# Kernel tuning notes

Hardware: AMD Instinct MI355X
Metric: run time of the kernel (lower is better)

The kernel has to match this reference:

```python
import jax, jax.numpy as jnp
import numpy as np

B, LQ, LKV, D = 4, 4096, 256, 1024
H, KVH, HD = 16, 4, 64
ROPE_BASE = 10000.0


def rotate_half(x):
    x1, x2 = jnp.split(x, 2, axis=-1)
    return jnp.concatenate([-x2, x1], axis=-1)


def rope_cos_sin(seq_len, dim, dtype):
    inv_freq = 1.0 / (ROPE_BASE ** (jnp.arange(0, dim, 2, dtype=jnp.float32) / dim))
    t = jnp.arange(seq_len, dtype=jnp.float32)
    freqs = t[:, None] * inv_freq[None, :]            # (T, dim/2)
    emb = jnp.concatenate([freqs, freqs], axis=-1)    # (T, dim)
    return jnp.cos(emb).astype(dtype), jnp.sin(emb).astype(dtype)


def apply_rope_indexed(x, cos, sin, pos_ids):
    # x: (B, L, H, HD); cos/sin: (T, HD); pos_ids: (L,)
    c = cos[pos_ids][None, :, None, :]
    s = sin[pos_ids][None, :, None, :]
    return x * c + rotate_half(x) * s


def setup_inputs() -> dict:
    key = jax.random.key(0)
    ks = jax.random.split(key, 10)
    sd = 1.0 / np.sqrt(D)
    return {
        "patches": jax.random.normal(ks[0], (B, LQ, D), jnp.float32),
        "latents": jax.random.normal(ks[1], (B, LKV, D), jnp.float32),
        "Wq": jax.random.normal(ks[2], (D, H * HD), jnp.float32) * sd,
        "bq": jax.random.normal(ks[3], (H * HD,), jnp.float32) * sd,
        "Wk": jax.random.normal(ks[4], (D, KVH * HD), jnp.float32) * sd,
        "bk": jax.random.normal(ks[5], (KVH * HD,), jnp.float32) * sd,
        "Wv": jax.random.normal(ks[6], (D, KVH * HD), jnp.float32) * sd,
        "bv": jax.random.normal(ks[7], (KVH * HD,), jnp.float32) * sd,
        "Wo": jax.random.normal(ks[8], (D, D), jnp.float32) * sd,
        "bo": jax.random.normal(ks[9], (D,), jnp.float32) * sd,
        "num_frames": 16,
    }


def reference(patches, latents, Wq, bq, Wk, bk, Wv, bv, Wo, bo, num_frames):
    Bc, Lq, C = patches.shape
    Lkv = latents.shape[1]
    q = (patches @ Wq + bq).reshape(Bc, Lq, H, HD)
    k = (latents @ Wk + bk).reshape(Bc, Lkv, KVH, HD)
    v = (latents @ Wv + bv).reshape(Bc, Lkv, KVH, HD)

    if num_frames > 1:
        cos, sin = rope_cos_sin(num_frames, HD, q.dtype)
        q_idx = jnp.arange(Lq) // (Lq // num_frames)
        k_idx = jnp.arange(Lkv) // (Lkv // num_frames)
        q = apply_rope_indexed(q, cos, sin, q_idx)
        k = apply_rope_indexed(k, cos, sin, k_idx)

    # GQA: expand kv heads (repeat_interleave along head axis)
    k = jnp.repeat(k, H // KVH, axis=2)
    v = jnp.repeat(v, H // KVH, axis=2)

    scale = 1.0 / np.sqrt(HD)
    scores = jnp.einsum('bqhd,bkhd->bhqk', q, k) * scale
    probs = jax.nn.softmax(scores, axis=-1)
    out = jnp.einsum('bhqk,bkhd->bqhd', probs, v).reshape(Bc, Lq, C)
    return out @ Wo + bo
```

## Files before the change

kernel.cpp:

```cpp
#include <hip/hip_runtime.h>
#include <hip/hip_fp16.h>
#include <cstdint>

typedef _Float16 f16x8 __attribute__((ext_vector_type(8)));
typedef _Float16 f16x4 __attribute__((ext_vector_type(4)));
typedef float    f32x4 __attribute__((ext_vector_type(4)));
typedef float    f32x16 __attribute__((ext_vector_type(16)));

#define MFMA16(a, b, c) __builtin_amdgcn_mfma_f32_16x16x32_f16((a), (b), (c), 0, 0, 0)
#define MFMA32(a, b, c) __builtin_amdgcn_mfma_f32_32x32x16_f16((a), (b), (c), 0, 0, 0)


__device__ __forceinline__ void async_cp16(const _Float16* g, _Float16* l) {
    __builtin_amdgcn_global_load_lds(
        (const __attribute__((address_space(1))) void*)g,
        (__attribute__((address_space(3))) void*)l, 16, 0, 0);
}

__global__ __launch_bounds__(256) void cvt_all(const float4* __restrict__ patches,
                                               const float4* __restrict__ latents,
                                               f16x4* __restrict__ p16,
                                               f16x4* __restrict__ l16) {
    const long i = (long)blockIdx.x * 256 + threadIdx.x;
    const float4 v = (i < 4194304) ? patches[i] : latents[i - 4194304];
    f16x4 o;
    o[0] = (_Float16)v.x; o[1] = (_Float16)v.y;
    o[2] = (_Float16)v.z; o[3] = (_Float16)v.w;
    if (i < 4194304) p16[i] = o; else l16[i - 4194304] = o;
}

__global__ __launch_bounds__(256) void transpose_all(
    const float* __restrict__ Wq, const float* __restrict__ Wk,
    const float* __restrict__ Wv, const float* __restrict__ Wo,
    _Float16* __restrict__ WqT, _Float16* __restrict__ WkvT,
    _Float16* __restrict__ WoT) {
    const int z = blockIdx.z;
    const float* W;
    _Float16* WT;
    int Nd;
    if (z == 0)      { W = Wq; WT = WqT;                       Nd = 1024; }
    else if (z == 1) { W = Wk; WT = WkvT;                      Nd = 256;  }
    else if (z == 2) { W = Wv; WT = WkvT + (size_t)256 * 1024; Nd = 256;  }
    else             { W = Wo; WT = WoT;                       Nd = 1024; }
    const int n0 = blockIdx.x * 64, k0 = blockIdx.y * 64;
    if (n0 >= Nd) return;

    __shared__ float T[64][65];
    const int tid = threadIdx.x;
    const int nl = tid & 63, kg = tid >> 6;
#pragma unroll
    for (int i = 0; i < 16; ++i) {
        const int kl = kg * 16 + i;
        T[kl][nl] = W[(size_t)(k0 + kl) * Nd + n0 + nl];
    }
    __syncthreads();
    const int kl = tid & 63;
#pragma unroll
    for (int i = 0; i < 16; ++i) {
        const int nl2 = kg * 16 + i;
        WT[(size_t)(n0 + nl2) * 1024 + k0 + kl] = (_Float16)T[kl][nl2];
    }
}

__global__ void catbias(const float* __restrict__ a, const float* __restrict__ b,
                        float* __restrict__ o) {
    const int i = threadIdx.x;
    o[i] = (i < 256) ? a[i] : b[i - 256];
}

template <int EPI>
__global__ __launch_bounds__(256, 2) void gemm32(const _Float16* __restrict__ A,
                                                 const _Float16* __restrict__ BT,
                                                 const float* __restrict__ bias,
                                                 void* __restrict__ Cp,
                                                 const int* __restrict__ nfp) {
    constexpr int K = 1024;
    __shared__ _Float16 As[256 * 64];
    __shared__ _Float16 Bs[128 * 64];

    const int tid = threadIdx.x;
    const int lane = tid & 63, l31 = lane & 31, hh = lane >> 5;
    const int w = tid >> 6, wm = w >> 1, wn = w & 1;

    constexpr int GXS = (EPI == 1) ? 2 : 3;
    constexpr int NWG = (EPI == 1) ? 16 : 512;
    int lin = (blockIdx.y << GXS) + blockIdx.x;
    lin = (lin & 7) * (NWG >> 3) + (lin >> 3);
    const int n0 = (lin & ((1 << GXS) - 1)) * 128;
    const int m0 = (lin >> GXS) * 256;

    f32x16 acc[4][2];
#pragma unroll
    for (int mt = 0; mt < 4; ++mt)
#pragma unroll
        for (int nt = 0; nt < 2; ++nt)
#pragma unroll
            for (int v = 0; v < 16; ++v) acc[mt][nt][v] = 0.f;

    for (int k0 = 0; k0 < K; k0 += 64) {
#pragma unroll
        for (int i = 0; i < 8; ++i) {
            const int id = i * 256 + tid;
            const int r = id >> 3;
            const int c = (id & 7) ^ (r & 7);
            async_cp16(A + (size_t)(m0 + r) * K + k0 + c * 8,
                       As + i * 2048 + w * 512);
        }
#pragma unroll
        for (int i = 0; i < 4; ++i) {
            const int id = i * 256 + tid;
            const int r = id >> 3;
            const int c = (id & 7) ^ (r & 7);
            async_cp16(BT + (size_t)(n0 + r) * K + k0 + c * 8,
                       Bs + i * 2048 + w * 512);
        }
        __syncthreads();

#pragma unroll
        for (int kk = 0; kk < 4; ++kk) {
            f16x8 af[4], bf[2];
#pragma unroll
            for (int mt = 0; mt < 4; ++mt) {
                const int row = wm * 128 + mt * 32 + l31;
                const int pc = (kk * 2 + hh) ^ (row & 7);
                af[mt] = *(const f16x8*)&As[row * 64 + pc * 8];
            }
#pragma unroll
            for (int nt = 0; nt < 2; ++nt) {
                const int row = wn * 64 + nt * 32 + l31;
                const int pc = (kk * 2 + hh) ^ (row & 7);
                bf[nt] = *(const f16x8*)&Bs[row * 64 + pc * 8];
            }
#pragma unroll
            for (int mt = 0; mt < 4; ++mt)
#pragma unroll
                for (int nt = 0; nt < 2; ++nt)
                    acc[mt][nt] = MFMA32(af[mt], bf[nt], acc[mt][nt]);
        }
        __syncthreads();
    }

    const int nf = nfp[0];
    const int nbase = n0 + wn * 64;

    float bb[2];
#pragma unroll
    for (int nt = 0; nt < 2; ++nt) bb[nt] = bias[nbase + nt * 32 + l31];
#pragma unroll
    for (int mt = 0; mt < 4; ++mt)
#pragma unroll
        for (int nt = 0; nt < 2; ++nt)
#pragma unroll
            for (int v = 0; v < 16; ++v) acc[mt][nt][v] += bb[nt];

    if constexpr (EPI == 0) {
        const float l2b = 13.287712379549449f;
        const float inv = exp2f(-((float)l31 * (1.0f / 32.0f)) * l2b);
        const int dv = 4096 / (nf > 1 ? nf : 1);
        _Float16* O = (_Float16*)Cp;
        const int head = nbase >> 6;
#pragma unroll
        for (int mt = 0; mt < 4; ++mt) {
#pragma unroll
            for (int v = 0; v < 16; ++v) {
                const int m = m0 + wm * 128 + mt * 32 + (v & 3) + 8 * (v >> 2) + 4 * hh;
                const int b = m >> 12, lq = m & 4095;
                if (nf > 1) {
                    const int pos = lq / dv;
                    float s, c;
                    __sincosf((float)pos * inv, &s, &c);
                    const float x1 = acc[mt][0][v], x2 = acc[mt][1][v];
                    acc[mt][0][v] = x1 * c - x2 * s;
                    acc[mt][1][v] = x2 * c + x1 * s;
                }
#pragma unroll
                for (int nt = 0; nt < 2; ++nt) {
                    const int hd = nt * 32 + l31;
                    O[(((size_t)(b * 16 + head)) * 4096 + lq) * 64 + hd] =
                        (_Float16)(acc[mt][nt][v] * 0.125f);
                }
            }
        }
    } else if constexpr (EPI == 1) {
        _Float16* kout = (_Float16*)Cp;
        _Float16* vout = kout + (size_t)4 * 4 * 256 * 64;
        if (nbase < 256) {
            const float l2b = 13.287712379549449f;
            const float inv = exp2f(-((float)l31 * (1.0f / 32.0f)) * l2b);
            const int dv = 256 / (nf > 1 ? nf : 1);
            const int kvh = nbase >> 6;
#pragma unroll
            for (int mt = 0; mt < 4; ++mt) {
#pragma unroll
                for (int v = 0; v < 16; ++v) {
                    const int m = m0 + wm * 128 + mt * 32 + (v & 3) + 8 * (v >> 2) + 4 * hh;
                    const int b = m >> 8, lkv = m & 255;
                    if (nf > 1) {
                        const int pos = lkv / dv;
                        float s, c;
                        __sincosf((float)pos * inv, &s, &c);
                        const float x1 = acc[mt][0][v], x2 = acc[mt][1][v];
                        acc[mt][0][v] = x1 * c - x2 * s;
                        acc[mt][1][v] = x2 * c + x1 * s;
                    }
#pragma unroll
                    for (int nt = 0; nt < 2; ++nt) {
                        const int hd = nt * 32 + l31;
                        kout[(((size_t)(b * 4 + kvh)) * 256 + lkv) * 64 + hd] =
                            (_Float16)acc[mt][nt][v];
                    }
                }
            }
        } else {
            const int kvh = (nbase - 256) >> 6;
#pragma unroll
            for (int mt = 0; mt < 4; ++mt) {
#pragma unroll
                for (int v = 0; v < 16; ++v) {
                    const int m = m0 + wm * 128 + mt * 32 + (v & 3) + 8 * (v >> 2) + 4 * hh;
                    const int b = m >> 8, lkv = m & 255;
                    const int s = (lkv & 0xE0) | ((lkv & 12) << 1) |
                                  ((lkv & 16) >> 2) | (lkv & 3);
#pragma unroll
                    for (int nt = 0; nt < 2; ++nt) {
                        const int hd = nt * 32 + l31;
                        vout[(((size_t)(b * 4 + kvh)) * 64 + hd) * 256 + s] =
                            (_Float16)acc[mt][nt][v];
                    }
                }
            }
        }
    } else {
        float* O = (float*)Cp;
#pragma unroll
        for (int mt = 0; mt < 4; ++mt) {
#pragma unroll
            for (int v = 0; v < 16; ++v) {
                const int m = m0 + wm * 128 + mt * 32 + (v & 3) + 8 * (v >> 2) + 4 * hh;
#pragma unroll
                for (int nt = 0; nt < 2; ++nt)
                    O[(size_t)m * 1024 + nbase + nt * 32 + l31] = acc[mt][nt][v];
            }
        }
    }
}

__global__ __launch_bounds__(512, 4) void attn5(const _Float16* __restrict__ qh,
                                                const _Float16* __restrict__ kh,
                                                const _Float16* __restrict__ vp,
                                                _Float16* __restrict__ attn) {
    __shared__ _Float16 Ks[256 * 64];
    __shared__ _Float16 Vs[64 * 256];

    const int tid = threadIdx.x;
    const int w = tid >> 6, lane = tid & 63, quad = lane >> 4, l15 = lane & 15;
    const int bh = blockIdx.x, b = bh >> 4, h = bh & 15, kvh = h >> 2;
    const int q0 = blockIdx.y * 512;

    const _Float16* kb = kh + (size_t)(b * 4 + kvh) * 256 * 64;
    const _Float16* vb = vp + (size_t)(b * 4 + kvh) * 64 * 256;
    const _Float16* qb = qh + ((size_t)bh * 4096 + q0) * 64;

#pragma unroll
    for (int i = 0; i < 4; ++i) {
        const int id = i * 512 + tid;
        const int r = id >> 3;
        const int c = (id & 7) ^ (r & 7);
        async_cp16(kb + (size_t)r * 64 + c * 8, Ks + i * 4096 + w * 512);
    }
#pragma unroll
    for (int i = 0; i < 4; ++i) {
        const int id = i * 512 + tid;
        const int hd = id >> 5;
        const int s5 = id & 31;
        const int c = s5 ^ ((hd & 7) << 2);
        async_cp16(vb + (size_t)hd * 256 + c * 8, Vs + i * 4096 + w * 512);
    }
    __syncthreads();

    const int sw = l15 & 7;
    const int p0 = quad ^ sw;
    const int vsw = sw << 2;
    const int crot = w & 3;

    const _Float16* qpre = qb + (size_t)(w * 64 + crot * 16 + l15) * 64 + quad * 8;
    f16x8 bq0 = *(const f16x8*)qpre;
    f16x8 bq1 = *(const f16x8*)(qpre + 32);

#pragma unroll 1
    for (int cc = 0; cc < 4; ++cc) {
        const int chunk = (cc + crot) & 3;
        const int qrow = w * 64 + chunk * 16;

        const int nchunk = (cc + 1 + crot) & 3;
        const _Float16* np = qb + (size_t)(w * 64 + nchunk * 16 + l15) * 64 + quad * 8;
        const f16x8 nq0 = *(const f16x8*)np;
        const f16x8 nq1 = *(const f16x8*)(np + 32);

        f32x4 st[16];
#pragma unroll
        for (int t = 0; t < 16; ++t)
#pragma unroll
            for (int rr = 0; rr < 4; ++rr) st[t][rr] = 0.f;

#pragma unroll
        for (int t = 0; t < 16; ++t) {
            const int row = t * 16 + l15;
            const f16x8 ka0 = *(const f16x8*)&Ks[row * 64 + p0 * 8];
            const f16x8 ka1 = *(const f16x8*)&Ks[row * 64 + (p0 ^ 4) * 8];
            st[t] = MFMA16(ka0, bq0, st[t]);
            st[t] = MFMA16(ka1, bq1, st[t]);
        }

        float rm = -1e30f;
#pragma unroll
        for (int t = 0; t < 16; ++t)
#pragma unroll
            for (int rr = 0; rr < 4; ++rr) rm = fmaxf(rm, st[t][rr]);
        rm = fmaxf(rm, __shfl_xor(rm, 16, 64));
        rm = fmaxf(rm, __shfl_xor(rm, 32, 64));

        float rs = 0.f;
#pragma unroll
        for (int t = 0; t < 16; ++t) {
#pragma unroll
            for (int rr = 0; rr < 4; ++rr) {
                st[t][rr] = __expf(st[t][rr] - rm);
                rs += st[t][rr];
            }
        }
        rs += __shfl_xor(rs, 16, 64);
        rs += __shfl_xor(rs, 32, 64);
        const float ir = 1.0f / rs;

        int vo = 0;
        asm volatile("" : "+v"(vo));

        f32x4 o[4];
#pragma unroll
        for (int nt = 0; nt < 4; ++nt)
#pragma unroll
            for (int rr = 0; rr < 4; ++rr) o[nt][rr] = 0.f;

#pragma unroll
        for (int c = 0; c < 8; ++c) {
            f16x8 pb;
#pragma unroll
            for (int j = 0; j < 8; ++j)
                pb[j] = (_Float16)st[2 * c + (j >> 2)][j & 3];
#pragma unroll
            for (int nt = 0; nt < 4; ++nt) {
                const f16x8 va = *(const f16x8*)&Vs[(nt * 16 + l15) * 256 +
                                                   (((c * 4 + quad) ^ vsw) * 8) + vo];
                o[nt] = MFMA16(va, pb, o[nt]);
            }
        }

        const size_t rowbase = ((size_t)b * 4096 + q0 + qrow + l15) * 1024 + h * 64;
#pragma unroll
        for (int nt = 0; nt < 4; ++nt) {
            f16x4 ov;
#pragma unroll
            for (int rr = 0; rr < 4; ++rr) ov[rr] = (_Float16)(o[nt][rr] * ir);
            *(f16x4*)&attn[rowbase + nt * 16 + quad * 4] = ov;
        }

        bq0 = nq0; bq1 = nq1;
    }
}

extern "C" void kernel_launch(void* const* d_in, const int* in_sizes, int n_in,
                              void* d_out, int out_size, void* d_ws, size_t ws_size,
                              hipStream_t stream) {
    const float* patches = (const float*)d_in[0];
    const float* latents = (const float*)d_in[1];
    const float* Wq = (const float*)d_in[2];
    const float* bq = (const float*)d_in[3];
    const float* Wk = (const float*)d_in[4];
    const float* bk = (const float*)d_in[5];
    const float* Wv = (const float*)d_in[6];
    const float* bv = (const float*)d_in[7];
    const float* Wo = (const float*)d_in[8];
    const float* bo = (const float*)d_in[9];
    const int*   nf = (const int*)d_in[10];
    float* out = (float*)d_out;
    (void)in_sizes; (void)n_in; (void)out_size; (void)ws_size;

    char* p = (char*)d_ws;
    _Float16* WqT  = (_Float16*)p; p += (size_t)1024 * 1024 * 2;
    _Float16* WkvT = (_Float16*)p; p += (size_t)512 * 1024 * 2;
    _Float16* WoT  = (_Float16*)p; p += (size_t)1024 * 1024 * 2;
    float*    bkv  = (float*)p;    p += 4096;
    _Float16* p16  = (_Float16*)p; p += (size_t)4 * 4096 * 1024 * 2;
    _Float16* l16  = (_Float16*)p; p += (size_t)4 * 256 * 1024 * 2;
    _Float16* q_h  = (_Float16*)p; p += (size_t)4 * 16 * 4096 * 64 * 2;
    _Float16* k_h  = (_Float16*)p; p += (size_t)4 * 4 * 256 * 64 * 2;
    _Float16* v_pi = (_Float16*)p; p += (size_t)4 * 4 * 256 * 64 * 2;
    _Float16* attn_h = (_Float16*)p; p += (size_t)16384 * 1024 * 2;

    cvt_all<<<17408, 256, 0, stream>>>((const float4*)patches, (const float4*)latents,
                                       (f16x4*)p16, (f16x4*)l16);
    transpose_all<<<dim3(16, 16, 4), 256, 0, stream>>>(Wq, Wk, Wv, Wo, WqT, WkvT, WoT);
    catbias<<<1, 512, 0, stream>>>(bk, bv, bkv);

    gemm32<1><<<dim3(4, 4), 256, 0, stream>>>(l16, WkvT, bkv, k_h, nf);
    gemm32<0><<<dim3(8, 64), 256, 0, stream>>>(p16, WqT, bq, q_h, nf);

    attn5<<<dim3(64, 8), 512, 0, stream>>>(q_h, k_h, v_pi, attn_h);

    gemm32<2><<<dim3(8, 64), 256, 0, stream>>>(attn_h, WoT, bo, out, nf);
}
```

Before: 299.4 us.

## Replace Q/O projection GEMMs with 256x256 8-wave pipelined MFMA16 kernel

Adds a new GEMM kernel with 512 threads and 256x256 tiles. It double-buffers A and B halves in LDS and interleaves async global-to-LDS copies with four MFMA16 quadrant phases, using explicit barriers, vmcnt waits and setprio. The kernel is used for the Q projection (with fused RoPE and scale) and the output projection. The old gemm32 is left handling only the KV projection, and its swizzled block ordering is removed. The aim is better data reuse and overlap of loads with compute. The price is a hand-managed schedule that is fragile and has a large register footprint.

```diff
diff --git a/kernel.cpp b/kernel.cpp
--- a/kernel.cpp
+++ b/kernel.cpp
@@ -82,12 +82,8 @@
     const int lane = tid & 63, l31 = lane & 31, hh = lane >> 5;
     const int w = tid >> 6, wm = w >> 1, wn = w & 1;
 
-    constexpr int GXS = (EPI == 1) ? 2 : 3;
-    constexpr int NWG = (EPI == 1) ? 16 : 512;
-    int lin = (blockIdx.y << GXS) + blockIdx.x;
-    lin = (lin & 7) * (NWG >> 3) + (lin >> 3);
-    const int n0 = (lin & ((1 << GXS) - 1)) * 128;
-    const int m0 = (lin >> GXS) * 256;
+    const int n0 = blockIdx.x * 128;
+    const int m0 = blockIdx.y * 256;
 
     f32x16 acc[4][2];
 #pragma unroll
@@ -153,35 +149,7 @@
 #pragma unroll
             for (int v = 0; v < 16; ++v) acc[mt][nt][v] += bb[nt];
 
-    if constexpr (EPI == 0) {
-        const float l2b = 13.287712379549449f;
-        const float inv = exp2f(-((float)l31 * (1.0f / 32.0f)) * l2b);
-        const int dv = 4096 / (nf > 1 ? nf : 1);
-        _Float16* O = (_Float16*)Cp;
-        const int head = nbase >> 6;
-#pragma unroll
-        for (int mt = 0; mt < 4; ++mt) {
-#pragma unroll
-            for (int v = 0; v < 16; ++v) {
-                const int m = m0 + wm * 128 + mt * 32 + (v & 3) + 8 * (v >> 2) + 4 * hh;
-                const int b = m >> 12, lq = m & 4095;
-                if (nf > 1) {
-                    const int pos = lq / dv;
-                    float s, c;
-                    __sincosf((float)pos * inv, &s, &c);
-                    const float x1 = acc[mt][0][v], x2 = acc[mt][1][v];
-                    acc[mt][0][v] = x1 * c - x2 * s;
-                    acc[mt][1][v] = x2 * c + x1 * s;
-                }
-#pragma unroll
-                for (int nt = 0; nt < 2; ++nt) {
-                    const int hd = nt * 32 + l31;
-                    O[(((size_t)(b * 16 + head)) * 4096 + lq) * 64 + hd] =
-                        (_Float16)(acc[mt][nt][v] * 0.125f);
-                }
-            }
-        }
-    } else if constexpr (EPI == 1) {
+    {
         _Float16* kout = (_Float16*)Cp;
         _Float16* vout = kout + (size_t)4 * 4 * 256 * 64;
         if (nbase < 256) {
@@ -230,19 +198,191 @@
                 }
             }
         }
+    }
+}
+
+template <int EPI>
+__global__ __launch_bounds__(512, 2) void gemm8p(const _Float16* __restrict__ A,
+                                                 const _Float16* __restrict__ BT,
+                                                 const float* __restrict__ bias,
+                                                 void* __restrict__ Cp,
+                                                 const int* __restrict__ nfp) {
+    constexpr int K = 1024;
+    __shared__ alignas(16) _Float16 lds[2][2][2][128 * 64];
+
+    const int tid = threadIdx.x;
+    const int lane = tid & 63, quad = lane >> 4, l15 = lane & 15;
+    const int w = tid >> 6, wm = w >> 2, wn = w & 3;
+
+    int lin = blockIdx.x;
+    lin = (lin & 7) * 32 + (lin >> 3);
+    const int m0 = (lin >> 2) * 256;
+    const int n0 = (lin & 3) * 256;
+
+    f32x4 acc[8][4];
+#pragma unroll
+    for (int mf = 0; mf < 8; ++mf)
+#pragma unroll
+        for (int nf = 0; nf < 4; ++nf)
+#pragma unroll
+            for (int rr = 0; rr < 4; ++rr) acc[mf][nf][rr] = 0.f;
+
+    f16x8 ra[4][2], rb[4][2];
+
+#define STAGE(BUF, MAT, HALF, KK0)                                              \
+    {                                                                           \
+        const _Float16* g_ = (MAT) ? BT : A;                                    \
+        const int rb_ = ((MAT) ? n0 : m0) + (HALF) * 128;                       \
+        _Float16* dst_ = &lds[BUF][MAT][HALF][0];                               \
+        _Pragma("unroll") for (int i_ = 0; i_ < 2; ++i_) {                      \
+            const int id_ = i_ * 512 + tid;                                     \
+            const int r_ = id_ >> 3;                                            \
+            const int c_ = (id_ & 7) ^ (r_ & 7);                                \
+            async_cp16(g_ + (size_t)(rb_ + r_) * K + (KK0) + c_ * 8,            \
+                       dst_ + i_ * 4096 + w * 512);                             \
+        }                                                                       \
+    }
+
+#define LDA4(BUF, MH)                                                           \
+    _Pragma("unroll") for (int i_ = 0; i_ < 4; ++i_)                            \
+    _Pragma("unroll") for (int ks_ = 0; ks_ < 2; ++ks_) {                       \
+        const int row_ = ((MH) * 4 + i_) * 16 + l15;                            \
+        ra[i_][ks_] = *(const f16x8*)&lds[BUF][0][wm]                           \
+            [row_ * 64 + (((ks_ * 4 + quad) ^ (l15 & 7)) * 8)];                 \
+    }
+
+#define LDB2(BUF, NFROM)                                                        \
+    _Pragma("unroll") for (int j_ = 0; j_ < 2; ++j_)                            \
+    _Pragma("unroll") for (int ks_ = 0; ks_ < 2; ++ks_) {                       \
+        const int nf_ = (NFROM) + j_;                                           \
+        const int row_ = (wn & 1) * 64 + nf_ * 16 + l15;                        \
+        rb[nf_][ks_] = *(const f16x8*)&lds[BUF][1][wn >> 1]                     \
+            [row_ * 64 + (((ks_ * 4 + quad) ^ (l15 & 7)) * 8)];                 \
+    }
+
+#define QUAD(QM, QN)                                                            \
+    {                                                                           \
+        __builtin_amdgcn_s_setprio(1);                                          \
+        _Pragma("unroll") for (int i_ = 0; i_ < 4; ++i_)                        \
+        _Pragma("unroll") for (int j_ = 0; j_ < 2; ++j_)                        \
+        _Pragma("unroll") for (int ks_ = 0; ks_ < 2; ++ks_)                     \
+            acc[(QM) * 4 + i_][(QN) * 2 + j_] =                                 \
+                MFMA16(ra[i_][ks_], rb[(QN) * 2 + j_][ks_],                     \
+                       acc[(QM) * 4 + i_][(QN) * 2 + j_]);                      \
+        __builtin_amdgcn_s_setprio(0);                                          \
+    }
+
+#define FENCE() asm volatile("" ::: "memory")
+#define BARR()  FENCE(); __builtin_amdgcn_s_barrier(); FENCE()
+#define LGKM0() asm volatile("s_waitcnt lgkmcnt(0)" ::: "memory");              \
+                __builtin_amdgcn_sched_barrier(0)
+#define VMC4()  asm volatile("s_waitcnt vmcnt(4)" ::: "memory")
+
+    STAGE(0, 1, 0, 0);
+    STAGE(0, 1, 1, 0);
+    STAGE(0, 0, 0, 0);
+    STAGE(0, 0, 1, 0);
+    STAGE(1, 1, 0, 64);
+    STAGE(1, 0, 0, 64);
+    VMC4();
+    BARR();
+
+    int k0 = 0;
+#pragma unroll 1
+    for (int it = 0; it < 8; ++it) {
+        const int k_t1 = k0 + 64;
+        const int k_n0 = (k0 + 128 < K) ? k0 + 128 : K - 64;
+        const int k_n1 = (k0 + 192 < K) ? k0 + 192 : K - 64;
+        LDA4(0, 0); LDB2(0, 0);
+        STAGE(1, 1, 1, k_t1);
+        BARR(); LGKM0(); QUAD(0, 0); BARR();
+        LDB2(0, 2);
+        STAGE(1, 0, 1, k_t1);
+        BARR(); LGKM0(); QUAD(0, 1); BARR();
+        LDA4(0, 1);
+        STAGE(0, 1, 0, k_n0);
+        BARR(); LGKM0(); QUAD(1, 0); BARR();
+        STAGE(0, 1, 1, k_n0);
+        BARR(); LGKM0(); QUAD(1, 1); VMC4(); BARR();
+        LDA4(1, 0); LDB2(1, 0);
+        STAGE(0, 0, 0, k_n0);
+        BARR(); LGKM0(); QUAD(0, 0); BARR();
+        LDB2(1, 2);
+        STAGE(0, 0, 1, k_n0);
+        BARR(); LGKM0(); QUAD(0, 1); BARR();
+        LDA4(1, 1);
+        STAGE(1, 1, 0, k_n1);
+        BARR(); LGKM0(); QUAD(1, 0); BARR();
+        STAGE(1, 0, 0, k_n1);
+        BARR(); LGKM0(); QUAD(1, 1); VMC4(); BARR();
+        k0 += 128;
+    }
+    asm volatile("s_waitcnt vmcnt(0)" ::: "memory");
+
+    const int nf_frames = nfp[0];
+    float bb[4];
+#pragma unroll
+    for (int nf = 0; nf < 4; ++nf) bb[nf] = bias[n0 + wn * 64 + nf * 16 + l15];
+#pragma unroll
+    for (int mf = 0; mf < 8; ++mf)
+#pragma unroll
+        for (int nf = 0; nf < 4; ++nf)
+#pragma unroll
+            for (int rr = 0; rr < 4; ++rr) acc[mf][nf][rr] += bb[nf];
+
+    if constexpr (EPI == 0) {
+        const float l2b = 13.287712379549449f;
+        const float inv0 = exp2f(-((float)l15 * (1.0f / 32.0f)) * l2b);
+        const float inv1 = exp2f(-((float)(16 + l15) * (1.0f / 32.0f)) * l2b);
+        const int dv = 4096 / (nf_frames > 1 ? nf_frames : 1);
+        _Float16* O = (_Float16*)Cp;
+        const int head = (n0 + wn * 64) >> 6;
+#pragma unroll
+        for (int mf = 0; mf < 8; ++mf) {
+#pragma unroll
+            for (int rr = 0; rr < 4; ++rr) {
+                const int m = m0 + wm * 128 + mf * 16 + quad * 4 + rr;
+                const int b = m >> 12, lq = m & 4095;
+                if (nf_frames > 1) {
+                    const int pos = lq / dv;
+                    float s0, c0, s1, c1;
+                    __sincosf((float)pos * inv0, &s0, &c0);
+                    __sincosf((float)pos * inv1, &s1, &c1);
+                    const float x0 = acc[mf][0][rr], x2 = acc[mf][2][rr];
+                    const float x1 = acc[mf][1][rr], x3 = acc[mf][3][rr];
+                    acc[mf][0][rr] = x0 * c0 - x2 * s0;
+                    acc[mf][2][rr] = x2 * c0 + x0 * s0;
+                    acc[mf][1][rr] = x1 * c1 - x3 * s1;
+                    acc[mf][3][rr] = x3 * c1 + x1 * s1;
+                }
+                const size_t base = (((size_t)(b * 16 + head)) * 4096 + lq) * 64;
+#pragma unroll
+                for (int nf = 0; nf < 4; ++nf)
+                    O[base + nf * 16 + l15] = (_Float16)(acc[mf][nf][rr] * 0.125f);
+            }
+        }
     } else {
         float* O = (float*)Cp;
 #pragma unroll
-        for (int mt = 0; mt < 4; ++mt) {
-#pragma unroll
-            for (int v = 0; v < 16; ++v) {
-                const int m = m0 + wm * 128 + mt * 32 + (v & 3) + 8 * (v >> 2) + 4 * hh;
-#pragma unroll
-                for (int nt = 0; nt < 2; ++nt)
-                    O[(size_t)m * 1024 + nbase + nt * 32 + l31] = acc[mt][nt][v];
-            }
-        }
-    }
+        for (int mf = 0; mf < 8; ++mf) {
+#pragma unroll
+            for (int rr = 0; rr < 4; ++rr) {
+                const int m = m0 + wm * 128 + mf * 16 + quad * 4 + rr;
+#pragma unroll
+                for (int nf = 0; nf < 4; ++nf)
+                    O[(size_t)m * 1024 + n0 + wn * 64 + nf * 16 + l15] =
+                        acc[mf][nf][rr];
+            }
+        }
+    }
+#undef STAGE
+#undef LDA4
+#undef LDB2
+#undef QUAD
+#undef FENCE
+#undef BARR
+#undef LGKM0
+#undef VMC4
 }
 
 __global__ __launch_bounds__(512, 4) void attn5(const _Float16* __restrict__ qh,
@@ -404,9 +544,9 @@
     catbias<<<1, 512, 0, stream>>>(bk, bv, bkv);
 
     gemm32<1><<<dim3(4, 4), 256, 0, stream>>>(l16, WkvT, bkv, k_h, nf);
-    gemm32<0><<<dim3(8, 64), 256, 0, stream>>>(p16, WqT, bq, q_h, nf);
+    gemm8p<0><<<256, 512, 0, stream>>>(p16, WqT, bq, q_h, nf);
 
     attn5<<<dim3(64, 8), 512, 0, stream>>>(q_h, k_h, v_pi, attn_h);
 
-    gemm32<2><<<dim3(8, 64), 256, 0, stream>>>(attn_h, WoT, bo, out, nf);
-}
+    gemm8p<2><<<256, 512, 0, stream>>>(attn_h, WoT, bo, out, nf);
+}
```

Result: faster. 284.6 us (-4.9%).
